# Optimization experiments

Measured on AMD Instinct MI355X. Metric: run time of the kernel, lower is better.

Reference implementation:

```python
import jax, jax.numpy as jnp
import numpy as np

EMBED_DIM = 2048
NUM_HEADS = 16
HEAD_DIM = EMBED_DIM // NUM_HEADS
BASE = 10000.0


def rotate_half(x):
    half = x.shape[-1] // 2
    x1, x2 = x[..., :half], x[..., half:]
    return jnp.concatenate([-x2, x1], axis=-1)


def apply_rope(x, base=BASE):
    # x: [B, H, S, Dh]
    S, Dh = x.shape[-2], x.shape[-1]
    inv_freq = 1.0 / (base ** (jnp.arange(0, Dh, 2, dtype=jnp.float32) / Dh))
    t = jnp.arange(S, dtype=jnp.float32)
    freqs = jnp.einsum('i,j->ij', t, inv_freq)          # [S, Dh/2]
    emb = jnp.concatenate([freqs, freqs], axis=-1)      # [S, Dh]
    return x * jnp.cos(emb) + rotate_half(x) * jnp.sin(emb)


def setup_inputs() -> dict:
    key = jax.random.key(0)
    ks = jax.random.split(key, 9)
    B, S, D = 2, 2048, EMBED_DIM
    xavier = lambda k, shape: jax.random.uniform(
        k, shape, jnp.float32, -1.0, 1.0) * float(np.sqrt(6.0 / (shape[0] + shape[1])))
    return {
        'x': jax.random.normal(ks[0], (B, S, D), jnp.float32),
        'q_w': xavier(ks[1], (D, D)),
        'k_w': xavier(ks[2], (D, D)),
        'v_w': xavier(ks[3], (D, D)),
        'q_b': jnp.zeros((D,), jnp.float32),
        'k_b': jnp.zeros((D,), jnp.float32),
        'v_b': jnp.zeros((D,), jnp.float32),
        'out_w': xavier(ks[4], (D, D)),
        'out_b': jnp.zeros((D,), jnp.float32),
    }


def reference(x, q_w, k_w, v_w, q_b, k_b, v_b, out_w, out_b):
    B, S, D = x.shape
    H, Dh = NUM_HEADS, HEAD_DIM
    scaling = Dh ** -0.5
    # F.linear(x, W, b) = x @ W.T + b
    q = (x @ q_w.T + q_b).reshape(B, S, H, Dh).transpose(0, 2, 1, 3)
    k = (x @ k_w.T + k_b).reshape(B, S, H, Dh).transpose(0, 2, 1, 3)
    v = (x @ v_w.T + v_b).reshape(B, S, H, Dh).transpose(0, 2, 1, 3)
    q = apply_rope(q)
    k = apply_rope(k)
    attn = jnp.einsum('bhqd,bhkd->bhqk', q, k) * scaling
    probs = jax.nn.softmax(attn, axis=-1)
    out = jnp.einsum('bhqk,bhkd->bhqd', probs, v)
    out = out.transpose(0, 2, 1, 3).reshape(B, S, D)
    return out @ out_w.T + out_b
```

## Files before the change

### kernel.cpp

```cpp
#include <hip/hip_runtime.h>
#include <stdint.h>

typedef __bf16 bf16;
typedef __bf16 bf16x4 __attribute__((ext_vector_type(4)));
typedef __bf16 bf16x8 __attribute__((ext_vector_type(8)));
typedef float f32x4 __attribute__((ext_vector_type(4)));
typedef float f32x16 __attribute__((ext_vector_type(16)));

#define DM 2048
#define MM 4096
#define MFMA16(a, b, c) __builtin_amdgcn_mfma_f32_16x16x32_bf16(a, b, c, 0, 0, 0)
#define MFMA32(a, b, c) __builtin_amdgcn_mfma_f32_32x32x16_bf16(a, b, c, 0, 0, 0)

#define WAITV_BAR(N) asm volatile("s_waitcnt vmcnt(" #N ")\n\ts_barrier" ::: "memory")
#define BAR()        asm volatile("s_barrier" ::: "memory")

__device__ __forceinline__ void gload_lds16(const void* g, void* l) {
  __builtin_amdgcn_global_load_lds((const __attribute__((address_space(1))) uint32_t*)g,
                                   (__attribute__((address_space(3))) uint32_t*)l, 16, 0, 0);
}

__global__ __launch_bounds__(256) void cvt_f32_bf16(
    const float* __restrict__ s0, const float* __restrict__ s1,
    const float* __restrict__ s2, const float* __restrict__ s3,
    const float* __restrict__ s4,
    bf16* __restrict__ d0, bf16* __restrict__ d1, bf16* __restrict__ d2,
    bf16* __restrict__ d3, bf16* __restrict__ d4)
{
  const size_t i4 = (size_t)(blockIdx.x * 256 + threadIdx.x) * 4;
  const float* s; bf16* d; size_t off;
  if      (i4 <  8388608u) { s = s0; d = d0; off = i4;             }
  else if (i4 < 12582912u) { s = s1; d = d1; off = i4 -  8388608u; }
  else if (i4 < 16777216u) { s = s2; d = d2; off = i4 - 12582912u; }
  else if (i4 < 20971520u) { s = s3; d = d3; off = i4 - 16777216u; }
  else                     { s = s4; d = d4; off = i4 - 20971520u; }
  const float4 v = *(const float4*)(s + off);
  bf16x4 o = { (bf16)v.x, (bf16)v.y, (bf16)v.z, (bf16)v.w };
  *(bf16x4*)(d + off) = o;
}

__global__ __launch_bounds__(256, 2) void gemm_qkv_fused(
    const bf16* __restrict__ A,
    const bf16* __restrict__ Wq, const bf16* __restrict__ Wk, const bf16* __restrict__ Wv,
    const float* __restrict__ qb, const float* __restrict__ kb, const float* __restrict__ vb,
    bf16* __restrict__ Cq, bf16* __restrict__ Ck, bf16* __restrict__ Cv)
{
  __shared__ __align__(16) bf16 smem[32768];
  bf16* As = smem;
  bf16* Ws = smem + 8192;

  const int id = blockIdx.x;
  const int xcd = id & 7, jj = id >> 3;
  const int n0 = (xcd * 2 + (jj >> 5)) * 128;
  const int m0 = (jj & 31) * 128;

  const int t = threadIdx.x;
  const int wave = t >> 6, lane = t & 63;
  const int quad = lane >> 4, c16 = lane & 15;
  const int wr = wave >> 1, wc = wave & 1;

  f32x4 acc[3][4][4] = {};

  const int srow = t >> 3;
  const int scol = ((t & 7) ^ (srow & 7)) * 8;
  const bf16* gA  = A  + (size_t)(m0 + srow) * DM + scol;
  const bf16* gW0 = Wq + (size_t)(n0 + srow) * DM + scol;
  const bf16* gW1 = Wk + (size_t)(n0 + srow) * DM + scol;
  const bf16* gW2 = Wv + (size_t)(n0 + srow) * DM + scol;

  for (int k0 = 0; k0 < DM; k0 += 64) {
#pragma unroll
    for (int rr = 0; rr < 4; ++rr) {
      const size_t go = (size_t)(rr * 32) * DM;
      const int lo = (rr * 256 + wave * 64) * 8;
      gload_lds16(gA  + go, As + lo);
      gload_lds16(gW0 + go, Ws + lo);
      gload_lds16(gW1 + go, Ws + 8192 + lo);
      gload_lds16(gW2 + go, Ws + 16384 + lo);
    }
    gA += 64; gW0 += 64; gW1 += 64; gW2 += 64;
    __syncthreads();

#pragma unroll
    for (int ks = 0; ks < 2; ++ks) {
      bf16x8 af[4];
#pragma unroll
      for (int i = 0; i < 4; ++i) {
        const int row = wr * 64 + i * 16 + c16;
        const int gi = (ks * 4 + quad) ^ (row & 7);
        af[i] = *(const bf16x8*)&As[row * 64 + gi * 8];
      }
#pragma unroll
      for (int z = 0; z < 3; ++z) {
        bf16x8 bfr[4];
#pragma unroll
        for (int jx = 0; jx < 4; ++jx) {
          const int row = wc * 64 + jx * 16 + c16;
          const int gi = (ks * 4 + quad) ^ (row & 7);
          bfr[jx] = *(const bf16x8*)&Ws[z * 8192 + row * 64 + gi * 8];
        }
#pragma unroll
        for (int i = 0; i < 4; ++i)
#pragma unroll
          for (int jx = 0; jx < 4; ++jx)
            acc[z][i][jx] = MFMA16(af[i], bfr[jx], acc[z][i][jx]);
      }
    }
    __syncthreads();
  }

  const int h = n0 >> 7;
#pragma unroll
  for (int jx = 0; jx < 4; ++jx) {
    const int d = wc * 64 + jx * 16 + c16;
    const float bv = vb[n0 + d];
#pragma unroll
    for (int i = 0; i < 4; ++i) {
      const int row = m0 + wr * 64 + i * 16 + quad * 4;
      const int b = row >> 11, s = row & 2047;
      bf16x4 o;
#pragma unroll
      for (int r = 0; r < 4; ++r) o[r] = (bf16)(acc[2][i][jx][r] + bv);
      *(bf16x4*)&Cv[((size_t)((b * 16 + h) * 128 + d)) * 2048 + s] = o;
    }
  }

  bf16* Tl = smem;
#pragma unroll
  for (int z = 0; z < 2; ++z) {
    __syncthreads();
#pragma unroll
    for (int jx = 0; jx < 4; ++jx) {
      const int col = wc * 64 + jx * 16 + c16;
      const float bv = (z == 0 ? qb : kb)[n0 + col];
#pragma unroll
      for (int i = 0; i < 4; ++i) {
        const int row = wr * 64 + i * 16 + quad * 4;
#pragma unroll
        for (int r = 0; r < 4; ++r)
          Tl[(row + r) * 136 + col] = (bf16)(acc[z][i][jx][r] + bv);
      }
    }
    __syncthreads();
    bf16* C = (z == 0) ? Cq : Ck;
    const float scale = (z == 0) ? 0.08838834764831845f * 1.4426950408889634f : 1.0f;
#pragma unroll
    for (int rr = 0; rr < 4; ++rr) {
      const int row = rr * 32 + (t >> 3);
      const int d0 = (t & 7) * 8;
      const int s = (m0 + row) & 2047;
      bf16x8 xa = *(const bf16x8*)&Tl[row * 136 + d0];
      bf16x8 xb = *(const bf16x8*)&Tl[row * 136 + d0 + 64];
      bf16x8 o1, o2;
#pragma unroll
      for (int j = 0; j < 8; ++j) {
        const float inv_freq = __expf((float)(d0 + j) * -0.14391156514261228f);
        float sn, cs;
        __sincosf((float)s * inv_freq, &sn, &cs);
        const float a = (float)xa[j], bb = (float)xb[j];
        o1[j] = (bf16)((a * cs - bb * sn) * scale);
        o2[j] = (bf16)((bb * cs + a * sn) * scale);
      }
      *(bf16x8*)&C[(size_t)(m0 + row) * DM + n0 + d0]      = o1;
      *(bf16x8*)&C[(size_t)(m0 + row) * DM + n0 + d0 + 64] = o2;
    }
  }
}

__global__ __launch_bounds__(256, 2) void gemm_bias_f32(
    const bf16* __restrict__ A, const bf16* __restrict__ W,
    const float* __restrict__ bias, float* __restrict__ C)
{
  __shared__ __align__(16) bf16 As[8192];
  __shared__ __align__(16) bf16 Bs[8192];
  const int id = blockIdx.x;
  const int xcd = id & 7, jj = id >> 3;
  const int n0 = (xcd * 2 + (jj >> 5)) * 128;
  const int m0 = (jj & 31) * 128;

  const int t = threadIdx.x;
  const int wave = t >> 6, lane = t & 63;
  const int quad = lane >> 4, c16 = lane & 15;
  const int wr = wave >> 1, wc = wave & 1;

  f32x4 acc[4][4] = {};
  const int srow = t >> 3;
  const int scol = ((t & 7) ^ (srow & 7)) * 8;
  const bf16* gA = A + (size_t)(m0 + srow) * DM + scol;
  const bf16* gB = W + (size_t)(n0 + srow) * DM + scol;

  for (int k0 = 0; k0 < DM; k0 += 64) {
#pragma unroll
    for (int rr = 0; rr < 4; ++rr) {
      const size_t go = (size_t)(rr * 32) * DM;
      const int lo = (rr * 256 + wave * 64) * 8;
      gload_lds16(gA + go, As + lo);
      gload_lds16(gB + go, Bs + lo);
    }
    gA += 64; gB += 64;
    __syncthreads();

#pragma unroll
    for (int ks = 0; ks < 2; ++ks) {
      bf16x8 af[4], bfr[4];
#pragma unroll
      for (int i = 0; i < 4; ++i) {
        const int row = wr * 64 + i * 16 + c16;
        const int gi = (ks * 4 + quad) ^ (row & 7);
        af[i] = *(const bf16x8*)&As[row * 64 + gi * 8];
      }
#pragma unroll
      for (int jx = 0; jx < 4; ++jx) {
        const int row = wc * 64 + jx * 16 + c16;
        const int gi = (ks * 4 + quad) ^ (row & 7);
        bfr[jx] = *(const bf16x8*)&Bs[row * 64 + gi * 8];
      }
#pragma unroll
      for (int i = 0; i < 4; ++i)
#pragma unroll
        for (int jx = 0; jx < 4; ++jx)
          acc[i][jx] = MFMA16(af[i], bfr[jx], acc[i][jx]);
    }
    __syncthreads();
  }

#pragma unroll
  for (int jx = 0; jx < 4; ++jx) {
    const int col = n0 + wc * 64 + jx * 16 + c16;
    const float bv = bias[col];
#pragma unroll
    for (int i = 0; i < 4; ++i) {
      const int row = m0 + wr * 64 + i * 16 + quad * 4;
#pragma unroll
      for (int r = 0; r < 4; ++r)
        C[(size_t)(row + r) * DM + col] = acc[i][jx][r] + bv;
    }
  }
}

__global__ __launch_bounds__(256, 1) void attn(
    const bf16* __restrict__ Q, const bf16* __restrict__ K,
    const bf16* __restrict__ Vt, bf16* __restrict__ O)
{
  __shared__ __align__(16) bf16 Ks[2][64][128];
  __shared__ __align__(16) bf16 Vs[2][128][64];
  const int t = threadIdx.x;
  const int wave = t >> 6, lane = t & 63;
  const int r31 = lane & 31, h = lane >> 5;
  const int id = blockIdx.x;
  const int xcd = id & 7, jj = id >> 3;
  const int bh = xcd * 4 + (jj >> 3);
  const int q0 = (jj & 7) * 256;
  const int b = bh >> 4, hd = bh & 15;

  bf16x8 qf[2][8];
#pragma unroll
  for (int qs = 0; qs < 2; ++qs) {
    const bf16* qrow = Q + (size_t)(b * 2048 + q0 + wave * 64 + qs * 32 + r31) * 2048
                         + (size_t)hd * 128 + h * 8;
#pragma unroll
    for (int ks = 0; ks < 8; ++ks) qf[qs][ks] = *(const bf16x8*)(qrow + ks * 16);
  }

  float l_i[2] = {0.f, 0.f};
  f32x16 o_acc[2][4] = {};

  const bf16* Kg = K + (size_t)(b * 2048) * 2048 + (size_t)hd * 128;
  const bf16* Vg = Vt + (size_t)bh * 128 * 2048;

  auto stage = [&](int kt0, int nb) {
#pragma unroll
    for (int rr = 0; rr < 4; ++rr) {
      const int G = rr * 256 + t;
      const int key = G >> 4, gl = G & 15;
      gload_lds16(Kg + (size_t)(kt0 + key) * 2048 + ((gl ^ (key & 7)) * 8),
                  (bf16*)Ks[nb] + (rr * 256 + wave * 64) * 8);
    }
#pragma unroll
    for (int rr = 0; rr < 4; ++rr) {
      const int G = rr * 256 + t;
      const int d = G >> 3, gl = G & 7;
      gload_lds16(Vg + (size_t)d * 2048 + kt0 + ((gl ^ (d & 7)) * 8),
                  (bf16*)Vs[nb] + (rr * 256 + wave * 64) * 8);
    }
  };

  stage(0, 0);

  for (int kt = 0; kt < 32; ++kt) {
    const int cb = kt & 1;
    if (kt < 31) {
      stage((kt + 1) * 64, cb ^ 1);
      WAITV_BAR(8);
    } else {
      WAITV_BAR(0);
    }

#pragma unroll
    for (int rb = 0; rb < 2; ++rb) {
      f32x16 st[2] = {};
#pragma unroll
      for (int ks = 0; ks < 8; ++ks) {
        const int key = rb * 32 + r31;
        const int g = (2 * ks + h) ^ (key & 7);
        bf16x8 kf = *(const bf16x8*)&Ks[cb][key][g * 8];
        st[0] = MFMA32(kf, qf[0][ks], st[0]);
        st[1] = MFMA32(kf, qf[1][ks], st[1]);
      }

      uint32_t pf[2][2][4];
#pragma unroll
      for (int qs = 0; qs < 2; ++qs) {
        float p[16];
#pragma unroll
        for (int r = 0; r < 16; ++r) { p[r] = exp2f(st[qs][r]); l_i[qs] += p[r]; }
        uint32_t pka[4], pkb[4];
#pragma unroll
        for (int pp = 0; pp < 4; ++pp) {
          asm("v_cvt_pk_bf16_f32 %0, %1, %2"
              : "=v"(pka[pp]) : "v"(p[4 * pp + 0]), "v"(p[4 * pp + 1]));
          asm("v_cvt_pk_bf16_f32 %0, %1, %2"
              : "=v"(pkb[pp]) : "v"(p[4 * pp + 2]), "v"(p[4 * pp + 3]));
        }
#pragma unroll
        for (int c = 0; c < 2; ++c) {
          uint32_t a0 = pka[2 * c], a1 = pka[2 * c + 1];
          uint32_t b0 = pkb[2 * c], b1 = pkb[2 * c + 1];
          asm("v_permlane32_swap_b32 %0, %1" : "+v"(a0), "+v"(a1));
          asm("v_permlane32_swap_b32 %0, %1" : "+v"(b0), "+v"(b1));
          pf[qs][c][0] = a0; pf[qs][c][1] = b0; pf[qs][c][2] = a1; pf[qs][c][3] = b1;
        }
      }

#pragma unroll
      for (int c = 0; c < 2; ++c) {
        const int kap = rb * 2 + c;
        union { uint32_t u[4]; bf16x8 v; } p0, p1;
#pragma unroll
        for (int w = 0; w < 4; ++w) { p0.u[w] = pf[0][c][w]; p1.u[w] = pf[1][c][w]; }
#pragma unroll
        for (int db = 0; db < 4; ++db) {
          const int d = db * 32 + r31;
          const int g = (2 * kap + h) ^ (d & 7);
          bf16x8 vf = *(const bf16x8*)&Vs[cb][d][g * 8];
          o_acc[0][db] = MFMA32(vf, p0.v, o_acc[0][db]);
          o_acc[1][db] = MFMA32(vf, p1.v, o_acc[1][db]);
        }
      }
    }
    BAR();
  }

#pragma unroll
  for (int qs = 0; qs < 2; ++qs) {
    float l = l_i[qs];
    l += __shfl_xor(l, 32, 64);
    const float invl = 1.0f / l;
    const int q = q0 + wave * 64 + qs * 32 + r31;
    bf16* orow = O + (size_t)(b * 2048 + q) * 2048 + (size_t)hd * 128;
#pragma unroll
    for (int db = 0; db < 4; ++db)
#pragma unroll
      for (int pp = 0; pp < 4; ++pp) {
        const int d0 = db * 32 + 8 * pp + 4 * h;
        bf16x4 o;
#pragma unroll
        for (int r = 0; r < 4; ++r) o[r] = (bf16)(o_acc[qs][db][4 * pp + r] * invl);
        *(bf16x4*)(orow + d0) = o;
      }
  }
}

extern "C" void kernel_launch(void* const* d_in, const int* in_sizes, int n_in,
                              void* d_out, int out_size, void* d_ws, size_t ws_size,
                              hipStream_t stream)
{
  (void)in_sizes; (void)n_in; (void)out_size; (void)ws_size;
  const float* x   = (const float*)d_in[0];
  const float* q_w = (const float*)d_in[1];
  const float* k_w = (const float*)d_in[2];
  const float* v_w = (const float*)d_in[3];
  const float* q_b = (const float*)d_in[4];
  const float* k_b = (const float*)d_in[5];
  const float* v_b = (const float*)d_in[6];
  const float* o_w = (const float*)d_in[7];
  const float* o_b = (const float*)d_in[8];

  const size_t NELEM = (size_t)MM * DM;
  const size_t WELEM = (size_t)DM * DM;
  bf16* Xb  = (bf16*)d_ws;
  bf16* Wq  = Xb + NELEM;
  bf16* Wk  = Wq + WELEM;
  bf16* Wv  = Wk + WELEM;
  bf16* Wo  = Wv + WELEM;
  bf16* Q   = Wo + WELEM;
  bf16* Kb  = Q  + NELEM;
  bf16* Vt  = Kb + NELEM;
  bf16* attnO = Xb;

  cvt_f32_bf16<<<24576, 256, 0, stream>>>(x, q_w, k_w, v_w, o_w, Xb, Wq, Wk, Wv, Wo);

  gemm_qkv_fused<<<512, 256, 0, stream>>>(Xb, Wq, Wk, Wv, q_b, k_b, v_b, Q, Kb, Vt);
  attn<<<256, 256, 0, stream>>>(Q, Kb, Vt, attnO);
  gemm_bias_f32<<<512, 256, 0, stream>>>(attnO, Wo, o_b, (float*)d_out);
}
```

Measured before the change: 378.1 us.

## Split attention keys across wave pairs and merge partial outputs in LDS

The attention kernel now processes 128 queries per block instead of 256, doubling the grid to 512 blocks. The four waves are split into two query groups times two key halves, and each wave handles 32 keys per step. At the end, partial O and row sums are combined through shared memory before normalising. This aims for better occupancy (launch bounds allow two blocks per CU) and load balance, at the cost of an LDS reduction epilogue and reloading Q for each block.

```diff
diff --git a/kernel.cpp b/kernel.cpp
--- a/kernel.cpp
+++ b/kernel.cpp
@@ -238,25 +238,25 @@
   }
 }
 
-__global__ __launch_bounds__(256, 1) void attn(
+__global__ __launch_bounds__(256, 2) void attn(
     const bf16* __restrict__ Q, const bf16* __restrict__ K,
     const bf16* __restrict__ Vt, bf16* __restrict__ O)
 {
-  __shared__ __align__(16) bf16 Ks[2][64][128];
-  __shared__ __align__(16) bf16 Vs[2][128][64];
+  __shared__ __align__(16) bf16 smem[32768];
   const int t = threadIdx.x;
   const int wave = t >> 6, lane = t & 63;
   const int r31 = lane & 31, h = lane >> 5;
+  const int qg = wave & 1, kh = wave >> 1;
   const int id = blockIdx.x;
   const int xcd = id & 7, jj = id >> 3;
-  const int bh = xcd * 4 + (jj >> 3);
-  const int q0 = (jj & 7) * 256;
+  const int bh = xcd * 4 + (jj >> 4);
+  const int q0 = (jj & 15) * 128;
   const int b = bh >> 4, hd = bh & 15;
 
   bf16x8 qf[2][8];
 #pragma unroll
   for (int qs = 0; qs < 2; ++qs) {
-    const bf16* qrow = Q + (size_t)(b * 2048 + q0 + wave * 64 + qs * 32 + r31) * 2048
+    const bf16* qrow = Q + (size_t)(b * 2048 + q0 + qg * 64 + qs * 32 + r31) * 2048
                          + (size_t)hd * 128 + h * 8;
 #pragma unroll
     for (int ks = 0; ks < 8; ++ks) qf[qs][ks] = *(const bf16x8*)(qrow + ks * 16);
@@ -268,106 +268,135 @@
   const bf16* Kg = K + (size_t)(b * 2048) * 2048 + (size_t)hd * 128;
   const bf16* Vg = Vt + (size_t)bh * 128 * 2048;
 
-  auto stage = [&](int kt0, int nb) {
-#pragma unroll
-    for (int rr = 0; rr < 4; ++rr) {
-      const int G = rr * 256 + t;
-      const int key = G >> 4, gl = G & 15;
-      gload_lds16(Kg + (size_t)(kt0 + key) * 2048 + ((gl ^ (key & 7)) * 8),
-                  (bf16*)Ks[nb] + (rr * 256 + wave * 64) * 8);
-    }
-#pragma unroll
-    for (int rr = 0; rr < 4; ++rr) {
-      const int G = rr * 256 + t;
-      const int d = G >> 3, gl = G & 7;
-      gload_lds16(Vg + (size_t)d * 2048 + kt0 + ((gl ^ (d & 7)) * 8),
-                  (bf16*)Vs[nb] + (rr * 256 + wave * 64) * 8);
+  auto stage = [&](int it, int nb) {
+#pragma unroll
+    for (int j = 0; j < 4; ++j) {
+      const int khs = j >> 1;
+      const int Gk = (j & 1) * 256 + t;
+      const int key = Gk >> 4, gl = Gk & 15;
+      gload_lds16(Kg + (size_t)(khs * 1024 + it * 32 + key) * 2048 + ((gl ^ (key & 7)) * 8),
+                  smem + khs * 8192 + nb * 4096 + ((j & 1) * 256 + wave * 64) * 8);
+    }
+#pragma unroll
+    for (int j = 0; j < 4; ++j) {
+      const int khs = j >> 1;
+      const int Gq = (j & 1) * 256 + t;
+      const int d = Gq >> 2, gl = Gq & 3;
+      gload_lds16(Vg + (size_t)d * 2048 + khs * 1024 + it * 32 + ((gl ^ (d & 3)) * 8),
+                  smem + 16384 + khs * 8192 + nb * 4096 + ((j & 1) * 256 + wave * 64) * 8);
     }
   };
 
   stage(0, 0);
 
-  for (int kt = 0; kt < 32; ++kt) {
-    const int cb = kt & 1;
-    if (kt < 31) {
-      stage((kt + 1) * 64, cb ^ 1);
+  for (int it = 0; it < 32; ++it) {
+    const int cb = it & 1;
+    if (it < 31) {
+      stage(it + 1, cb ^ 1);
       WAITV_BAR(8);
     } else {
       WAITV_BAR(0);
     }
 
-#pragma unroll
-    for (int rb = 0; rb < 2; ++rb) {
-      f32x16 st[2] = {};
-#pragma unroll
-      for (int ks = 0; ks < 8; ++ks) {
-        const int key = rb * 32 + r31;
-        const int g = (2 * ks + h) ^ (key & 7);
-        bf16x8 kf = *(const bf16x8*)&Ks[cb][key][g * 8];
-        st[0] = MFMA32(kf, qf[0][ks], st[0]);
-        st[1] = MFMA32(kf, qf[1][ks], st[1]);
-      }
-
-      uint32_t pf[2][2][4];
+    const bf16* KsB = smem + kh * 8192 + cb * 4096;
+    const bf16* VsB = smem + 16384 + kh * 8192 + cb * 4096;
+
+    f32x16 st[2] = {};
+#pragma unroll
+    for (int ks = 0; ks < 8; ++ks) {
+      const int g = (2 * ks + h) ^ (r31 & 7);
+      bf16x8 kf = *(const bf16x8*)&KsB[r31 * 128 + g * 8];
+      st[0] = MFMA32(kf, qf[0][ks], st[0]);
+      st[1] = MFMA32(kf, qf[1][ks], st[1]);
+    }
+
+    uint32_t pw[2][2][4];
+#pragma unroll
+    for (int qs = 0; qs < 2; ++qs) {
+      float p[16];
+#pragma unroll
+      for (int r = 0; r < 16; ++r) { p[r] = exp2f(st[qs][r]); l_i[qs] += p[r]; }
+      uint32_t pka[4], pkb[4];
+#pragma unroll
+      for (int pp = 0; pp < 4; ++pp) {
+        asm("v_cvt_pk_bf16_f32 %0, %1, %2"
+            : "=v"(pka[pp]) : "v"(p[4 * pp + 0]), "v"(p[4 * pp + 1]));
+        asm("v_cvt_pk_bf16_f32 %0, %1, %2"
+            : "=v"(pkb[pp]) : "v"(p[4 * pp + 2]), "v"(p[4 * pp + 3]));
+      }
+#pragma unroll
+      for (int c = 0; c < 2; ++c) {
+        uint32_t a0 = pka[2 * c], a1 = pka[2 * c + 1];
+        uint32_t b0 = pkb[2 * c], b1 = pkb[2 * c + 1];
+        asm("v_permlane32_swap_b32 %0, %1" : "+v"(a0), "+v"(a1));
+        asm("v_permlane32_swap_b32 %0, %1" : "+v"(b0), "+v"(b1));
+        pw[qs][c][0] = a0; pw[qs][c][1] = b0; pw[qs][c][2] = a1; pw[qs][c][3] = b1;
+      }
+    }
+
+#pragma unroll
+    for (int c = 0; c < 2; ++c) {
+      union { uint32_t u[4]; bf16x8 v; } p0, p1;
+#pragma unroll
+      for (int w2 = 0; w2 < 4; ++w2) { p0.u[w2] = pw[0][c][w2]; p1.u[w2] = pw[1][c][w2]; }
+      const int g = (2 * c + h) ^ (r31 & 3);
+#pragma unroll
+      for (int db = 0; db < 4; ++db) {
+        bf16x8 vf = *(const bf16x8*)&VsB[(db * 32 + r31) * 32 + g * 8];
+        o_acc[0][db] = MFMA32(vf, p0.v, o_acc[0][db]);
+        o_acc[1][db] = MFMA32(vf, p1.v, o_acc[1][db]);
+      }
+    }
+    BAR();
+  }
+
+  float lw[2];
+#pragma unroll
+  for (int qs = 0; qs < 2; ++qs) lw[qs] = l_i[qs] + __shfl_xor(l_i[qs], 32, 64);
+
+  float* fb = (float*)smem;
+  float* lb = fb + 8192;
+
+#pragma unroll
+  for (int ph = 0; ph < 2; ++ph) {
+    __syncthreads();
+    if (wave == 2 + ph) {
 #pragma unroll
       for (int qs = 0; qs < 2; ++qs) {
-        float p[16];
-#pragma unroll
-        for (int r = 0; r < 16; ++r) { p[r] = exp2f(st[qs][r]); l_i[qs] += p[r]; }
-        uint32_t pka[4], pkb[4];
-#pragma unroll
-        for (int pp = 0; pp < 4; ++pp) {
-          asm("v_cvt_pk_bf16_f32 %0, %1, %2"
-              : "=v"(pka[pp]) : "v"(p[4 * pp + 0]), "v"(p[4 * pp + 1]));
-          asm("v_cvt_pk_bf16_f32 %0, %1, %2"
-              : "=v"(pkb[pp]) : "v"(p[4 * pp + 2]), "v"(p[4 * pp + 3]));
-        }
-#pragma unroll
-        for (int c = 0; c < 2; ++c) {
-          uint32_t a0 = pka[2 * c], a1 = pka[2 * c + 1];
-          uint32_t b0 = pkb[2 * c], b1 = pkb[2 * c + 1];
-          asm("v_permlane32_swap_b32 %0, %1" : "+v"(a0), "+v"(a1));
-          asm("v_permlane32_swap_b32 %0, %1" : "+v"(b0), "+v"(b1));
-          pf[qs][c][0] = a0; pf[qs][c][1] = b0; pf[qs][c][2] = a1; pf[qs][c][3] = b1;
-        }
-      }
-
-#pragma unroll
-      for (int c = 0; c < 2; ++c) {
-        const int kap = rb * 2 + c;
-        union { uint32_t u[4]; bf16x8 v; } p0, p1;
-#pragma unroll
-        for (int w = 0; w < 4; ++w) { p0.u[w] = pf[0][c][w]; p1.u[w] = pf[1][c][w]; }
-#pragma unroll
-        for (int db = 0; db < 4; ++db) {
-          const int d = db * 32 + r31;
-          const int g = (2 * kap + h) ^ (d & 7);
-          bf16x8 vf = *(const bf16x8*)&Vs[cb][d][g * 8];
-          o_acc[0][db] = MFMA32(vf, p0.v, o_acc[0][db]);
-          o_acc[1][db] = MFMA32(vf, p1.v, o_acc[1][db]);
-        }
-      }
-    }
-    BAR();
-  }
-
-#pragma unroll
-  for (int qs = 0; qs < 2; ++qs) {
-    float l = l_i[qs];
-    l += __shfl_xor(l, 32, 64);
-    const float invl = 1.0f / l;
-    const int q = q0 + wave * 64 + qs * 32 + r31;
-    bf16* orow = O + (size_t)(b * 2048 + q) * 2048 + (size_t)hd * 128;
-#pragma unroll
-    for (int db = 0; db < 4; ++db)
-#pragma unroll
-      for (int pp = 0; pp < 4; ++pp) {
-        const int d0 = db * 32 + 8 * pp + 4 * h;
-        bf16x4 o;
-#pragma unroll
-        for (int r = 0; r < 4; ++r) o[r] = (bf16)(o_acc[qs][db][4 * pp + r] * invl);
-        *(bf16x4*)(orow + d0) = o;
-      }
+#pragma unroll
+        for (int db = 0; db < 4; ++db)
+#pragma unroll
+          for (int pp = 0; pp < 4; ++pp) {
+            float4 v = { o_acc[qs][db][4 * pp + 0], o_acc[qs][db][4 * pp + 1],
+                         o_acc[qs][db][4 * pp + 2], o_acc[qs][db][4 * pp + 3] };
+            *(float4*)&fb[lane * 128 + qs * 64 + db * 16 + pp * 4] = v;
+          }
+        lb[lane * 2 + qs] = lw[qs];
+      }
+    }
+    __syncthreads();
+    if (wave == ph) {
+#pragma unroll
+      for (int qs = 0; qs < 2; ++qs) {
+        const float l = lw[qs] + lb[lane * 2 + qs];
+        const float invl = 1.0f / l;
+        const int q = q0 + ph * 64 + qs * 32 + r31;
+        bf16* orow = O + (size_t)(b * 2048 + q) * 2048 + (size_t)hd * 128;
+#pragma unroll
+        for (int db = 0; db < 4; ++db)
+#pragma unroll
+          for (int pp = 0; pp < 4; ++pp) {
+            float4 v = *(const float4*)&fb[lane * 128 + qs * 64 + db * 16 + pp * 4];
+            const int d0 = db * 32 + 8 * pp + 4 * h;
+            bf16x4 o;
+            o[0] = (bf16)((o_acc[qs][db][4 * pp + 0] + v.x) * invl);
+            o[1] = (bf16)((o_acc[qs][db][4 * pp + 1] + v.y) * invl);
+            o[2] = (bf16)((o_acc[qs][db][4 * pp + 2] + v.z) * invl);
+            o[3] = (bf16)((o_acc[qs][db][4 * pp + 3] + v.w) * invl);
+            *(bf16x4*)(orow + d0) = o;
+          }
+      }
+    }
   }
 }
 
@@ -401,6 +430,6 @@
   cvt_f32_bf16<<<24576, 256, 0, stream>>>(x, q_w, k_w, v_w, o_w, Xb, Wq, Wk, Wv, Wo);
 
   gemm_qkv_fused<<<512, 256, 0, stream>>>(Xb, Wq, Wk, Wv, q_b, k_b, v_b, Q, Kb, Vt);
-  attn<<<256, 256, 0, stream>>>(Q, Kb, Vt, attnO);
+  attn<<<512, 256, 0, stream>>>(Q, Kb, Vt, attnO);
   gemm_bias_f32<<<512, 256, 0, stream>>>(attnO, Wo, o_b, (float*)d_out);
 }
```

Result: no change. 379.4 us (+0.3%).
